# Kernel tuning notes

Hardware: AMD Instinct MI355X
Metric: run time of the kernel (lower is better)

The kernel has to match this reference:

```python
import jax, jax.numpy as jnp
import numpy as np

BN_EPS = 1e-5

def _bn_relu(x, gamma, beta, mean, var):
    # x: [B, N, C]; BatchNorm1d(N) in eval mode normalizes over dim=1 (N)
    inv = jax.lax.rsqrt(var + BN_EPS)
    scale = (gamma * inv)[None, :, None]
    shift = (beta - mean * gamma * inv)[None, :, None]
    return jax.nn.relu(x * scale + shift)

def _forward(x, q_gamma, q_beta, q_mean, q_var,
             k_gamma, k_beta, k_mean, k_var,
             v_gamma, v_beta, v_mean, v_var,
             Wq, Wk, Wv, Wp):
    B, C, H, W = x.shape
    N = H * W
    E = Wq.shape[0]
    xs = x.reshape(B, C, N).transpose(0, 2, 1)  # [B, N, C]
    # BN+ReLU over spatial axis, then Linear(N->E) on spatial axis per channel -> [B, E, C]
    q = jnp.einsum('bnc,en->bec', _bn_relu(xs, q_gamma, q_beta, q_mean, q_var), Wq)
    k = jnp.einsum('bnc,en->bec', _bn_relu(xs, k_gamma, k_beta, k_mean, k_var), Wk)
    v = jnp.einsum('bnc,en->bec', _bn_relu(xs, v_gamma, v_beta, v_mean, v_var), Wv)
    scores = jnp.einsum('bec,bfc->bef', q, k) / jnp.sqrt(jnp.asarray(E, x.dtype))  # [B, E, E]
    attn = jax.nn.softmax(scores, axis=-1)
    out = jnp.einsum('bef,bfc->bec', attn, v)          # [B, E, C]
    out = jnp.einsum('bec,ne->bcn', out, Wp)            # Linear(E->N) -> [B, C, N]
    return out.reshape(B, C, H, W)

def setup_inputs() -> dict:
    key = jax.random.key(0)
    ks = jax.random.split(key, 20)
    B, C, H, W = 32, 512, 32, 32
    N = H * W  # sp_dim = 1024
    E = 1024   # embed_dim
    d = {'x': jax.random.normal(ks[0], (B, C, H, W), jnp.float32)}
    i = 1
    for p in ('q', 'k', 'v'):
        d[f'{p}_gamma'] = jax.random.uniform(ks[i], (N,), jnp.float32, 0.5, 1.5); i += 1
        d[f'{p}_beta'] = 0.1 * jax.random.normal(ks[i], (N,), jnp.float32); i += 1
        d[f'{p}_mean'] = 0.1 * jax.random.normal(ks[i], (N,), jnp.float32); i += 1
        d[f'{p}_var'] = jax.random.uniform(ks[i], (N,), jnp.float32, 0.5, 1.5); i += 1
    # torch Linear weight layout: [out, in]; scale ~ 1/sqrt(fan_in)
    d['Wq'] = jax.random.normal(ks[i], (E, N), jnp.float32) * (1.0 / np.sqrt(N)); i += 1
    d['Wk'] = jax.random.normal(ks[i], (E, N), jnp.float32) * (1.0 / np.sqrt(N)); i += 1
    d['Wv'] = jax.random.normal(ks[i], (E, N), jnp.float32) * (1.0 / np.sqrt(N)); i += 1
    d['Wp'] = jax.random.normal(ks[i], (N, E), jnp.float32) * (1.0 / np.sqrt(E)); i += 1
    return d

def reference(x, q_gamma, q_beta, q_mean, q_var,
              k_gamma, k_beta, k_mean, k_var,
              v_gamma, v_beta, v_mean, v_var,
              Wq, Wk, Wv, Wp):
    return _forward(x, q_gamma, q_beta, q_mean, q_var,
                    k_gamma, k_beta, k_mean, k_var,
                    v_gamma, v_beta, v_mean, v_var,
                    Wq, Wk, Wv, Wp)
```

## Files before the change

kernel.cpp:

```cpp
#include <hip/hip_runtime.h>
#include <math.h>

#define BN_EPS 1e-5f

namespace {

constexpr int Bb = 32;
constexpr int Cc = 512;
constexpr int Nn = 1024;
constexpr int Ee = 1024;

typedef __attribute__((ext_vector_type(8))) short short8;
typedef __attribute__((ext_vector_type(4))) float f32x4;
typedef __attribute__((ext_vector_type(4))) unsigned short ushort4_t;

struct bfpair { unsigned short h, l; };

__device__ __forceinline__ unsigned short bf16_rne(float v) {
  unsigned u = __builtin_bit_cast(unsigned, v);
  unsigned r = u + 0x7FFFu + ((u >> 16) & 1u);
  return (unsigned short)(r >> 16);
}
__device__ __forceinline__ float bf16_to_f(unsigned short h) {
  unsigned u = ((unsigned)h) << 16;
  return __builtin_bit_cast(float, u);
}
__device__ __forceinline__ bfpair split_bf(float v) {
  bfpair p;
  p.h = bf16_rne(v);
  p.l = bf16_rne(v - bf16_to_f(p.h));
  return p;
}

__device__ __forceinline__ void gll16(const void* g, void* l) {
  __builtin_amdgcn_global_load_lds(
      (const __attribute__((address_space(1))) void*)g,
      (__attribute__((address_space(3))) void*)l, 16, 0, 0);
}

__global__ __launch_bounds__(256) void prep3(
    const float* __restrict__ qg, const float* __restrict__ qb,
    const float* __restrict__ qm, const float* __restrict__ qv,
    const float* __restrict__ kg, const float* __restrict__ kb,
    const float* __restrict__ km, const float* __restrict__ kv,
    const float* __restrict__ vg, const float* __restrict__ vb,
    const float* __restrict__ vm, const float* __restrict__ vv,
    float* __restrict__ hdr) {
  int i = blockIdx.x * blockDim.x + threadIdx.x;
  if (i < 1024) {
    float inv, sc;
    inv = rsqrtf(qv[i] + BN_EPS); sc = qg[i] * inv;
    hdr[i] = sc;          hdr[1024 + i] = qb[i] - qm[i] * sc;
    inv = rsqrtf(kv[i] + BN_EPS); sc = kg[i] * inv;
    hdr[2048 + i] = sc;   hdr[3072 + i] = kb[i] - km[i] * sc;
    inv = rsqrtf(vv[i] + BN_EPS); sc = vg[i] * inv;
    hdr[4096 + i] = sc;   hdr[5120 + i] = vb[i] - vm[i] * sc;
  }
}

__global__ __launch_bounds__(256) void convert_w(
    const float* __restrict__ wsrc, unsigned short* __restrict__ wh,
    unsigned short* __restrict__ wl, long total4) {
  for (long i = (long)blockIdx.x * 256 + threadIdx.x; i < total4; i += (long)gridDim.x * 256) {
    float4 v = ((const float4*)wsrc)[i];
    bfpair p0 = split_bf(v.x), p1 = split_bf(v.y), p2 = split_bf(v.z), p3 = split_bf(v.w);
    ushort4_t hv, lv;
    hv.x = p0.h; hv.y = p1.h; hv.z = p2.h; hv.w = p3.h;
    lv.x = p0.l; lv.y = p1.l; lv.z = p2.l; lv.w = p3.l;
    *(ushort4_t*)&wh[i * 4] = hv;
    *(ushort4_t*)&wl[i * 4] = lv;
  }
}

__global__ __launch_bounds__(256) void convert_y3(
    const float* __restrict__ x, const float* __restrict__ hdr,
    unsigned short* __restrict__ yqh, unsigned short* __restrict__ yql,
    unsigned short* __restrict__ ykh, unsigned short* __restrict__ ykl,
    unsigned short* __restrict__ dout_us, long b0, long total4) {
  const float* sq = hdr;        const float* tq = hdr + 1024;
  const float* sk = hdr + 2048; const float* tk = hdr + 3072;
  const float* sv = hdr + 4096; const float* tv = hdr + 5120;
  for (long i = (long)blockIdx.x * 256 + threadIdx.x; i < total4; i += (long)gridDim.x * 256) {
    float4 v = ((const float4*)x)[i];
    int n4 = (int)(i & 255);
    float4 a, b;
    ushort4_t hv, lv;
    a = ((const float4*)sq)[n4]; b = ((const float4*)tq)[n4];
    {
      bfpair p0 = split_bf(fmaxf(fmaf(v.x, a.x, b.x), 0.f));
      bfpair p1 = split_bf(fmaxf(fmaf(v.y, a.y, b.y), 0.f));
      bfpair p2 = split_bf(fmaxf(fmaf(v.z, a.z, b.z), 0.f));
      bfpair p3 = split_bf(fmaxf(fmaf(v.w, a.w, b.w), 0.f));
      hv.x = p0.h; hv.y = p1.h; hv.z = p2.h; hv.w = p3.h;
      lv.x = p0.l; lv.y = p1.l; lv.z = p2.l; lv.w = p3.l;
      *(ushort4_t*)&yqh[i * 4] = hv; *(ushort4_t*)&yql[i * 4] = lv;
    }
    a = ((const float4*)sk)[n4]; b = ((const float4*)tk)[n4];
    {
      bfpair p0 = split_bf(fmaxf(fmaf(v.x, a.x, b.x), 0.f));
      bfpair p1 = split_bf(fmaxf(fmaf(v.y, a.y, b.y), 0.f));
      bfpair p2 = split_bf(fmaxf(fmaf(v.z, a.z, b.z), 0.f));
      bfpair p3 = split_bf(fmaxf(fmaf(v.w, a.w, b.w), 0.f));
      hv.x = p0.h; hv.y = p1.h; hv.z = p2.h; hv.w = p3.h;
      lv.x = p0.l; lv.y = p1.l; lv.z = p2.l; lv.w = p3.l;
      *(ushort4_t*)&ykh[i * 4] = hv; *(ushort4_t*)&ykl[i * 4] = lv;
    }
    a = ((const float4*)sv)[n4]; b = ((const float4*)tv)[n4];
    {
      bfpair p0 = split_bf(fmaxf(fmaf(v.x, a.x, b.x), 0.f));
      bfpair p1 = split_bf(fmaxf(fmaf(v.y, a.y, b.y), 0.f));
      bfpair p2 = split_bf(fmaxf(fmaf(v.z, a.z, b.z), 0.f));
      bfpair p3 = split_bf(fmaxf(fmaf(v.w, a.w, b.w), 0.f));
      hv.x = p0.h; hv.y = p1.h; hv.z = p2.h; hv.w = p3.h;
      lv.x = p0.l; lv.y = p1.l; lv.z = p2.l; lv.w = p3.l;
      long g = i >> 17;
      long local = i & 131071;
      unsigned short* slot = dout_us + (b0 + g) * 1048576L;
      *(ushort4_t*)&slot[local * 4] = hv;
      *(ushort4_t*)&slot[524288 + local * 4] = lv;
    }
  }
}

template<bool SPLIT, bool MFIRST, int BM>
__global__ __launch_bounds__(512, 2) void gemm3p(
    const unsigned short* __restrict__ Ah, const unsigned short* __restrict__ Al,
    long ldA, long bsA,
    const unsigned short* __restrict__ Bh0, const unsigned short* __restrict__ Bl0,
    const unsigned short* __restrict__ Bh1, const unsigned short* __restrict__ Bl1,
    int msel, long ldB, long bsB,
    float* __restrict__ Cf, unsigned short* __restrict__ Chi, unsigned short* __restrict__ Clo,
    long ldC, long bsC, int K, float alpha, int g0, int g1) {
  constexpr int WH = BM / 2;
  constexpr int AF = WH / 16;
  __shared__ unsigned short sA[2][2][BM][32];
  __shared__ unsigned short sB[2][2][256][32];

  const int nb = gridDim.x;
  int f = blockIdx.x;
  if ((nb & 7) == 0) f = (f & 7) * (nb >> 3) + (f >> 3);
  const int i0 = f % g0, i1 = (f / g0) % g1;
  const long zb = f / (g0 * g1);
  const int m0 = (MFIRST ? i0 : i1) * BM;
  const int n0 = (MFIRST ? i1 : i0) * 256;

  const int t = threadIdx.x, lane = t & 63, w = t >> 6;
  const int wr = w >> 2, wc = w & 3;
  const int sr  = lane >> 2;
  const int skc = (((lane & 3) ^ ((lane >> 3) & 3)) * 8);
  const int fr = lane & 15;
  const int kq = ((((lane >> 4) & 3) ^ ((fr >> 1) & 3)) * 8);

  const unsigned short* Bh = (m0 >= msel) ? Bh1 : Bh0;
  const unsigned short* Bl = (m0 >= msel) ? Bl1 : Bl0;

  const int aw = w & 3, ahl = w >> 2;
  const unsigned short* a0;
  const unsigned short* a1 = nullptr;
  if (BM == 256) {
    a0 = Ah + zb * bsA + (long)(m0 + w * 32 + sr) * ldA + skc;
    a1 = Al + zb * bsA + (long)(m0 + w * 32 + sr) * ldA + skc;
  } else {
    a0 = (ahl ? Al : Ah) + zb * bsA + (long)(m0 + aw * 32 + sr) * ldA + skc;
  }
  const unsigned short* b0 = Bh + zb * bsB + (long)(n0 + w * 32 + sr) * ldB + skc;
  const unsigned short* b1 = Bl + zb * bsB + (long)(n0 + w * 32 + sr) * ldB + skc;
  const long a16 = 16 * ldA, b16 = 16 * ldB;

  auto STAGE = [&](int buf) {
    if constexpr (BM == 256) {
      gll16(a0, &sA[buf][0][w * 32][0]);  gll16(a0 + a16, &sA[buf][0][w * 32 + 16][0]);
      gll16(a1, &sA[buf][1][w * 32][0]);  gll16(a1 + a16, &sA[buf][1][w * 32 + 16][0]);
      a0 += 32; a1 += 32;
    } else {
      gll16(a0, &sA[buf][ahl][aw * 32][0]);
      gll16(a0 + a16, &sA[buf][ahl][aw * 32 + 16][0]);
      a0 += 32;
    }
    gll16(b0, &sB[buf][0][w * 32][0]);  gll16(b0 + b16, &sB[buf][0][w * 32 + 16][0]);
    gll16(b1, &sB[buf][1][w * 32][0]);  gll16(b1 + b16, &sB[buf][1][w * 32 + 16][0]);
    b0 += 32; b1 += 32;
  };

  f32x4 acc[AF][4] = {};
  const int nt = K >> 5;

  STAGE(0);
  STAGE(1);
  int cur = 0;

  for (int it = 0; it < nt; ++it) {
    if (it + 1 < nt) {
      if constexpr (BM == 256) asm volatile("s_waitcnt vmcnt(8)" ::: "memory");
      else                     asm volatile("s_waitcnt vmcnt(6)" ::: "memory");
    } else {
      asm volatile("s_waitcnt vmcnt(0)" ::: "memory");
    }
    asm volatile("s_barrier" ::: "memory");

    short8 bh[4], bl[4], ah[4], al[4];
#pragma unroll
    for (int j = 0; j < 4; ++j) {
      bh[j] = *(const short8*)&sB[cur][0][wc * 64 + j * 16 + fr][kq];
      bl[j] = *(const short8*)&sB[cur][1][wc * 64 + j * 16 + fr][kq];
    }
#pragma unroll
    for (int i = 0; i < 4; ++i) {
      ah[i] = *(const short8*)&sA[cur][0][wr * WH + i * 16 + fr][kq];
      al[i] = *(const short8*)&sA[cur][1][wr * WH + i * 16 + fr][kq];
    }

    if constexpr (BM == 256) {
      __builtin_amdgcn_s_setprio(1);
#pragma unroll
      for (int i = 0; i < 4; ++i)
#pragma unroll
        for (int j = 0; j < 4; ++j) {
          acc[i][j] = __builtin_amdgcn_mfma_f32_16x16x32_bf16(ah[i], bh[j], acc[i][j], 0, 0, 0);
          acc[i][j] = __builtin_amdgcn_mfma_f32_16x16x32_bf16(ah[i], bl[j], acc[i][j], 0, 0, 0);
          acc[i][j] = __builtin_amdgcn_mfma_f32_16x16x32_bf16(al[i], bh[j], acc[i][j], 0, 0, 0);
        }
      __builtin_amdgcn_s_setprio(0);
#pragma unroll
      for (int i = 0; i < 4; ++i) {
        ah[i] = *(const short8*)&sA[cur][0][wr * WH + (i + 4) * 16 + fr][kq];
        al[i] = *(const short8*)&sA[cur][1][wr * WH + (i + 4) * 16 + fr][kq];
      }
      asm volatile("s_waitcnt lgkmcnt(0)" ::: "memory");
      asm volatile("s_barrier" ::: "memory");
      if (it + 2 < nt) STAGE(cur);
      __builtin_amdgcn_s_setprio(1);
#pragma unroll
      for (int i = 0; i < 4; ++i)
#pragma unroll
        for (int j = 0; j < 4; ++j) {
          acc[i + 4][j] = __builtin_amdgcn_mfma_f32_16x16x32_bf16(ah[i], bh[j], acc[i + 4][j], 0, 0, 0);
          acc[i + 4][j] = __builtin_amdgcn_mfma_f32_16x16x32_bf16(ah[i], bl[j], acc[i + 4][j], 0, 0, 0);
          acc[i + 4][j] = __builtin_amdgcn_mfma_f32_16x16x32_bf16(al[i], bh[j], acc[i + 4][j], 0, 0, 0);
        }
      __builtin_amdgcn_s_setprio(0);
    } else {
      asm volatile("s_waitcnt lgkmcnt(0)" ::: "memory");
      asm volatile("s_barrier" ::: "memory");
      if (it + 2 < nt) STAGE(cur);
      __builtin_amdgcn_s_setprio(1);
#pragma unroll
      for (int i = 0; i < 4; ++i)
#pragma unroll
        for (int j = 0; j < 4; ++j) {
          acc[i][j] = __builtin_amdgcn_mfma_f32_16x16x32_bf16(ah[i], bh[j], acc[i][j], 0, 0, 0);
          acc[i][j] = __builtin_amdgcn_mfma_f32_16x16x32_bf16(ah[i], bl[j], acc[i][j], 0, 0, 0);
          acc[i][j] = __builtin_amdgcn_mfma_f32_16x16x32_bf16(al[i], bh[j], acc[i][j], 0, 0, 0);
        }
      __builtin_amdgcn_s_setprio(0);
    }
    cur ^= 1;
  }

  const int rb = ((lane >> 4) & 3) * 4;
#pragma unroll
  for (int i = 0; i < AF; ++i)
#pragma unroll
    for (int j = 0; j < 4; ++j) {
      long col = n0 + wc * 64 + j * 16 + fr;
#pragma unroll
      for (int v = 0; v < 4; ++v) {
        long row = m0 + wr * WH + i * 16 + rb + v;
        float val = acc[i][j][v] * alpha;
        long idx = zb * bsC + row * ldC + col;
        if (SPLIT) {
          bfpair p = split_bf(val);
          Chi[idx] = p.h;
          Clo[idx] = p.l;
        } else {
          Cf[idx] = val;
        }
      }
    }
}

__global__ __launch_bounds__(256) void softmax_rows(float* __restrict__ S) {
  long row = blockIdx.x;
  float* p = S + row * 1024;
  int t = threadIdx.x;
  float4 v = *(float4*)(p + 4 * t);
  float mx = fmaxf(fmaxf(v.x, v.y), fmaxf(v.z, v.w));
#pragma unroll
  for (int i = 1; i < 64; i <<= 1) mx = fmaxf(mx, __shfl_xor(mx, i));
  __shared__ float redm[4];
  __shared__ float reds[4];
  int wave = t >> 6, lane = t & 63;
  if (lane == 0) redm[wave] = mx;
  __syncthreads();
  mx = fmaxf(fmaxf(redm[0], redm[1]), fmaxf(redm[2], redm[3]));
  float e0 = expf(v.x - mx), e1 = expf(v.y - mx);
  float e2 = expf(v.z - mx), e3 = expf(v.w - mx);
  float sum = (e0 + e1) + (e2 + e3);
#pragma unroll
  for (int i = 1; i < 64; i <<= 1) sum += __shfl_xor(sum, i);
  if (lane == 0) reds[wave] = sum;
  __syncthreads();
  sum = (reds[0] + reds[1]) + (reds[2] + reds[3]);
  float inv = 1.0f / sum;
  bfpair p0 = split_bf(e0 * inv), p1 = split_bf(e1 * inv);
  bfpair p2 = split_bf(e2 * inv), p3 = split_bf(e3 * inv);
  ushort4_t hv, lv;
  hv.x = p0.h; hv.y = p1.h; hv.z = p2.h; hv.w = p3.h;
  lv.x = p0.l; lv.y = p1.l; lv.z = p2.l; lv.w = p3.l;
  unsigned short* ph = (unsigned short*)p;
  *(ushort4_t*)&ph[4 * t] = hv;
  *(ushort4_t*)&ph[1024 + 4 * t] = lv;
}

}

extern "C" void kernel_launch(void* const* d_in, const int* in_sizes, int n_in,
                              void* d_out, int out_size, void* d_ws, size_t ws_size,
                              hipStream_t stream) {
  const float* x  = (const float*)d_in[0];
  const float* qg = (const float*)d_in[1];
  const float* qb = (const float*)d_in[2];
  const float* qm = (const float*)d_in[3];
  const float* qv = (const float*)d_in[4];
  const float* kg = (const float*)d_in[5];
  const float* kb = (const float*)d_in[6];
  const float* km = (const float*)d_in[7];
  const float* kv = (const float*)d_in[8];
  const float* vg = (const float*)d_in[9];
  const float* vb = (const float*)d_in[10];
  const float* vm = (const float*)d_in[11];
  const float* vv = (const float*)d_in[12];
  const float* Wq = (const float*)d_in[13];
  const float* Wk = (const float*)d_in[14];
  const float* Wv = (const float*)d_in[15];
  const float* Wp = (const float*)d_in[16];

  const size_t wFix = 65536 + 16UL * 1024 * 1024;
  const size_t perB = 12UL * 1024 * 1024;
  int G = 32;
  while (G > 1 && wFix + (size_t)G * perB > ws_size) G >>= 1;

  char* ws = (char*)d_ws;
  float* hdr = (float*)ws;

  const long WE = 1024L * 1024;
  unsigned short* WQKh = (unsigned short*)(ws + 65536);
  unsigned short* WQKl = WQKh + 2 * WE;
  unsigned short* Wvh  = WQKl + 2 * WE;
  unsigned short* Wvl  = Wvh + WE;
  unsigned short* Wph  = Wvl + WE;
  unsigned short* Wpl  = Wph + WE;

  const long YB = 524288;
  unsigned short* yqh = Wpl + WE;
  unsigned short* yql = yqh + (long)G * YB;
  unsigned short* ykh = yql + (long)G * YB;
  unsigned short* ykl = ykh + (long)G * YB;
  const long QKBS = 1048576;
  unsigned short* QKh = ykl + (long)G * YB;
  unsigned short* QKl = QKh + (long)G * QKBS;
  float* S = (float*)(QKl + (long)G * QKBS);

  unsigned short* dout_us = (unsigned short*)d_out;

  dim3 blk(256);
  const int BIG = 1 << 30;

  prep3<<<dim3(4), blk, 0, stream>>>(qg, qb, qm, qv, kg, kb, km, kv, vg, vb, vm, vv, hdr);

  const long W4 = WE / 4;
  convert_w<<<dim3(1024), blk, 0, stream>>>(Wq, WQKh, WQKl, W4);
  convert_w<<<dim3(1024), blk, 0, stream>>>(Wk, WQKh + WE, WQKl + WE, W4);
  convert_w<<<dim3(1024), blk, 0, stream>>>(Wv, Wvh, Wvl, W4);
  convert_w<<<dim3(1024), blk, 0, stream>>>(Wp, Wph, Wpl, W4);

  for (int b0 = 0; b0 < Bb; b0 += G) {
    const float* xg = x + (size_t)b0 * Cc * Nn;

    convert_y3<<<dim3(2048), blk, 0, stream>>>(
        xg, hdr, yqh, yql, ykh, ykl, dout_us, b0, (long)G * 131072);

    gemm3p<true, true, 256><<<dim3(8 * 2 * G), dim3(512), 0, stream>>>(
        WQKh, WQKl, Nn, 0L,
        yqh, yql, ykh, ykl, 1024, Nn, YB,
        nullptr, QKh, QKl, Cc, QKBS, Nn, 1.0f, 8, 2);

    gemm3p<false, false, 256><<<dim3(4 * 4 * G), dim3(512), 0, stream>>>(
        QKh, QKl, Cc, QKBS,
        QKh + 524288, QKl + 524288, nullptr, nullptr, BIG, Cc, QKBS,
        S, nullptr, nullptr, Ee, 1048576L, Cc, 0.03125f, 4, 4);

    softmax_rows<<<dim3(G * Ee), blk, 0, stream>>>(S);

    gemm3p<true, false, 128><<<dim3(4 * 4 * G), dim3(512), 0, stream>>>(
        dout_us + (long)b0 * 1048576, dout_us + (long)b0 * 1048576 + 524288, Nn, 1048576L,
        Wvh, Wvl, nullptr, nullptr, BIG, Nn, 0L,
        nullptr, yqh, yql, Ee, YB, Nn, 1.0f, 4, 4);

    gemm3p<true, false, 128><<<dim3(4 * 4 * G), dim3(512), 0, stream>>>(
        yqh, yql, Ee, YB,
        (unsigned short*)S, (unsigned short*)S + 1024, nullptr, nullptr, BIG,
        2L * Ee, 2097152L,
        nullptr, QKh, QKl, Ee, QKBS, Ee, 1.0f, 4, 4);

    gemm3p<false, false, 128><<<dim3(4 * 4 * G), dim3(512), 0, stream>>>(
        QKh, QKl, Ee, QKBS,
        Wph, Wpl, nullptr, nullptr, BIG, Ee, 0L,
        (float*)d_out + (size_t)b0 * Cc * Nn, nullptr, nullptr,
        Nn, (long)Cc * Nn, Ee, 1.0f, 4, 4);
  }
}
```

Baseline: 731.4 us.

## Split GEMM tile staging into halves interleaved with MFMA phases

The main loop of the 3-pass bf16 split GEMM is restructured. Each tile load is split into two halves, and the double buffer now prefetches one iteration ahead instead of two. The first half is issued at the top of the iteration and the second half after the first MFMA phase. A-fragment LDS reads are now done per pair of row-blocks just before their MFMAs, which lowers register pressure, with extra barriers between phases. The goal is finer interleaving of global-to-LDS traffic with matrix work, at the cost of a shorter prefetch distance and more barriers.

```diff
diff --git a/kernel.cpp b/kernel.cpp
--- a/kernel.cpp
+++ b/kernel.cpp
@@ -122,6 +122,27 @@
   }
 }
 
+#define MFMA_BF16 __builtin_amdgcn_mfma_f32_16x16x32_bf16
+
+#define PHASE_PAIR(I0)                                                        \
+  {                                                                           \
+    short8 ah0 = *(const short8*)&sA[cur][0][wr * WH + (I0) * 16 + fr][kq];   \
+    short8 al0 = *(const short8*)&sA[cur][1][wr * WH + (I0) * 16 + fr][kq];   \
+    short8 ah1 = *(const short8*)&sA[cur][0][wr * WH + (I0 + 1) * 16 + fr][kq]; \
+    short8 al1 = *(const short8*)&sA[cur][1][wr * WH + (I0 + 1) * 16 + fr][kq]; \
+    __builtin_amdgcn_s_setprio(1);                                            \
+    _Pragma("unroll")                                                         \
+    for (int j = 0; j < 4; ++j) {                                             \
+      acc[I0][j]     = MFMA_BF16(ah0, bh[j], acc[I0][j], 0, 0, 0);            \
+      acc[I0][j]     = MFMA_BF16(ah0, bl[j], acc[I0][j], 0, 0, 0);            \
+      acc[I0][j]     = MFMA_BF16(al0, bh[j], acc[I0][j], 0, 0, 0);            \
+      acc[I0 + 1][j] = MFMA_BF16(ah1, bh[j], acc[I0 + 1][j], 0, 0, 0);        \
+      acc[I0 + 1][j] = MFMA_BF16(ah1, bl[j], acc[I0 + 1][j], 0, 0, 0);        \
+      acc[I0 + 1][j] = MFMA_BF16(al1, bh[j], acc[I0 + 1][j], 0, 0, 0);        \
+    }                                                                         \
+    __builtin_amdgcn_s_setprio(0);                                            \
+  }
+
 template<bool SPLIT, bool MFIRST, int BM>
 __global__ __launch_bounds__(512, 2) void gemm3p(
     const unsigned short* __restrict__ Ah, const unsigned short* __restrict__ Al,
@@ -167,93 +188,67 @@
   const unsigned short* b1 = Bl + zb * bsB + (long)(n0 + w * 32 + sr) * ldB + skc;
   const long a16 = 16 * ldA, b16 = 16 * ldB;
 
-  auto STAGE = [&](int buf) {
+  auto STAGE_0 = [&](int buf) {
+    if constexpr (BM == 256) {
+      gll16(b0, &sB[buf][0][w * 32][0]);  gll16(b0 + b16, &sB[buf][0][w * 32 + 16][0]);
+      gll16(b1, &sB[buf][1][w * 32][0]);  gll16(b1 + b16, &sB[buf][1][w * 32 + 16][0]);
+      b0 += 32; b1 += 32;
+    } else {
+      gll16(a0, &sA[buf][ahl][aw * 32][0]);
+      gll16(b0, &sB[buf][0][w * 32][0]);
+      gll16(b1, &sB[buf][1][w * 32][0]);
+    }
+  };
+  auto STAGE_1 = [&](int buf) {
     if constexpr (BM == 256) {
       gll16(a0, &sA[buf][0][w * 32][0]);  gll16(a0 + a16, &sA[buf][0][w * 32 + 16][0]);
       gll16(a1, &sA[buf][1][w * 32][0]);  gll16(a1 + a16, &sA[buf][1][w * 32 + 16][0]);
       a0 += 32; a1 += 32;
     } else {
-      gll16(a0, &sA[buf][ahl][aw * 32][0]);
       gll16(a0 + a16, &sA[buf][ahl][aw * 32 + 16][0]);
-      a0 += 32;
-    }
-    gll16(b0, &sB[buf][0][w * 32][0]);  gll16(b0 + b16, &sB[buf][0][w * 32 + 16][0]);
-    gll16(b1, &sB[buf][1][w * 32][0]);  gll16(b1 + b16, &sB[buf][1][w * 32 + 16][0]);
-    b0 += 32; b1 += 32;
+      gll16(b0 + b16, &sB[buf][0][w * 32 + 16][0]);
+      gll16(b1 + b16, &sB[buf][1][w * 32 + 16][0]);
+      a0 += 32; b0 += 32; b1 += 32;
+    }
   };
 
   f32x4 acc[AF][4] = {};
   const int nt = K >> 5;
 
-  STAGE(0);
-  STAGE(1);
+  STAGE_0(0);
+  STAGE_1(0);
   int cur = 0;
 
   for (int it = 0; it < nt; ++it) {
-    if (it + 1 < nt) {
-      if constexpr (BM == 256) asm volatile("s_waitcnt vmcnt(8)" ::: "memory");
-      else                     asm volatile("s_waitcnt vmcnt(6)" ::: "memory");
+    const bool pf = (it + 1 < nt);
+    if (pf) {
+      STAGE_0(cur ^ 1);
+      if constexpr (BM == 256) asm volatile("s_waitcnt vmcnt(4)" ::: "memory");
+      else                     asm volatile("s_waitcnt vmcnt(3)" ::: "memory");
     } else {
       asm volatile("s_waitcnt vmcnt(0)" ::: "memory");
     }
     asm volatile("s_barrier" ::: "memory");
 
-    short8 bh[4], bl[4], ah[4], al[4];
+    short8 bh[4], bl[4];
 #pragma unroll
     for (int j = 0; j < 4; ++j) {
       bh[j] = *(const short8*)&sB[cur][0][wc * 64 + j * 16 + fr][kq];
       bl[j] = *(const short8*)&sB[cur][1][wc * 64 + j * 16 + fr][kq];
     }
-#pragma unroll
-    for (int i = 0; i < 4; ++i) {
-      ah[i] = *(const short8*)&sA[cur][0][wr * WH + i * 16 + fr][kq];
-      al[i] = *(const short8*)&sA[cur][1][wr * WH + i * 16 + fr][kq];
-    }
-
+
+    PHASE_PAIR(0)
+    asm volatile("s_barrier" ::: "memory");
+    if (pf) STAGE_1(cur ^ 1);
+    PHASE_PAIR(2)
     if constexpr (BM == 256) {
-      __builtin_amdgcn_s_setprio(1);
-#pragma unroll
-      for (int i = 0; i < 4; ++i)
-#pragma unroll
-        for (int j = 0; j < 4; ++j) {
-          acc[i][j] = __builtin_amdgcn_mfma_f32_16x16x32_bf16(ah[i], bh[j], acc[i][j], 0, 0, 0);
-          acc[i][j] = __builtin_amdgcn_mfma_f32_16x16x32_bf16(ah[i], bl[j], acc[i][j], 0, 0, 0);
-          acc[i][j] = __builtin_amdgcn_mfma_f32_16x16x32_bf16(al[i], bh[j], acc[i][j], 0, 0, 0);
-        }
-      __builtin_amdgcn_s_setprio(0);
-#pragma unroll
-      for (int i = 0; i < 4; ++i) {
-        ah[i] = *(const short8*)&sA[cur][0][wr * WH + (i + 4) * 16 + fr][kq];
-        al[i] = *(const short8*)&sA[cur][1][wr * WH + (i + 4) * 16 + fr][kq];
-      }
-      asm volatile("s_waitcnt lgkmcnt(0)" ::: "memory");
       asm volatile("s_barrier" ::: "memory");
-      if (it + 2 < nt) STAGE(cur);
-      __builtin_amdgcn_s_setprio(1);
-#pragma unroll
-      for (int i = 0; i < 4; ++i)
-#pragma unroll
-        for (int j = 0; j < 4; ++j) {
-          acc[i + 4][j] = __builtin_amdgcn_mfma_f32_16x16x32_bf16(ah[i], bh[j], acc[i + 4][j], 0, 0, 0);
-          acc[i + 4][j] = __builtin_amdgcn_mfma_f32_16x16x32_bf16(ah[i], bl[j], acc[i + 4][j], 0, 0, 0);
-          acc[i + 4][j] = __builtin_amdgcn_mfma_f32_16x16x32_bf16(al[i], bh[j], acc[i + 4][j], 0, 0, 0);
-        }
-      __builtin_amdgcn_s_setprio(0);
-    } else {
-      asm volatile("s_waitcnt lgkmcnt(0)" ::: "memory");
+      PHASE_PAIR(4)
       asm volatile("s_barrier" ::: "memory");
-      if (it + 2 < nt) STAGE(cur);
-      __builtin_amdgcn_s_setprio(1);
-#pragma unroll
-      for (int i = 0; i < 4; ++i)
-#pragma unroll
-        for (int j = 0; j < 4; ++j) {
-          acc[i][j] = __builtin_amdgcn_mfma_f32_16x16x32_bf16(ah[i], bh[j], acc[i][j], 0, 0, 0);
-          acc[i][j] = __builtin_amdgcn_mfma_f32_16x16x32_bf16(ah[i], bl[j], acc[i][j], 0, 0, 0);
-          acc[i][j] = __builtin_amdgcn_mfma_f32_16x16x32_bf16(al[i], bh[j], acc[i][j], 0, 0, 0);
-        }
-      __builtin_amdgcn_s_setprio(0);
-    }
+      PHASE_PAIR(6)
+    }
+    asm volatile("s_waitcnt lgkmcnt(0)" ::: "memory");
+    asm volatile("s_barrier" ::: "memory");
     cur ^= 1;
   }
 
```

New measurement: 842.9 us. 1.15x slower.
